# Kernel tuning notes

Hardware: AMD Instinct MI355X
Metric: run time of the kernel (lower is better)

The kernel has to match this reference:

```python
import math
import jax, jax.numpy as jnp
import numpy as np

HEADS = 8
DIM_HEAD = 64
NUM_MEM_KV = 16


def alibi_slopes(heads):
    def pow2_slopes(n):
        start = 2 ** (-(2 ** -(math.log2(n) - 3)))
        return [start * (start ** i) for i in range(n)]
    if math.log2(heads).is_integer():
        return np.asarray(pow2_slopes(heads), dtype=np.float32)
    cp2 = 2 ** math.floor(math.log2(heads))
    extra = pow2_slopes(2 * cp2)[0::2][: heads - cp2]
    return np.asarray(pow2_slopes(cp2) + extra, dtype=np.float32)


def setup_inputs() -> dict:
    key = jax.random.key(0)
    ks = jax.random.split(key, 12)
    b, n, dim = 2, 2048, 512
    h, dh, mem = HEADS, DIM_HEAD, NUM_MEM_KV
    s = 0.02  # weight init scale for numerical sanity
    return {
        "x": jax.random.normal(ks[0], (b, n, dim), jnp.float32),
        "Wq": jax.random.normal(ks[1], (dim, h * dh), jnp.float32) * s,
        "Wk": jax.random.normal(ks[2], (dim, h * dh), jnp.float32) * s,
        "Wv": jax.random.normal(ks[3], (dim, h * dh), jnp.float32) * s,
        "mem_k": jax.random.normal(ks[4], (h, mem, dh), jnp.float32),
        "mem_v": jax.random.normal(ks[5], (h, mem, dh), jnp.float32),
        "pre_proj": jax.random.normal(ks[6], (h, h), jnp.float32),
        "post_proj": jax.random.normal(ks[7], (h, h), jnp.float32),
        "head_scale_params": jnp.ones((1, h, 1, 1), jnp.float32),
        "Wout": jax.random.normal(ks[8], (h * dh, dim), jnp.float32) * s,
        "bout": jnp.zeros((dim,), jnp.float32),
    }


def reference(x, Wq, Wk, Wv, mem_k, mem_v, pre_proj, post_proj,
              head_scale_params, Wout, bout):
    b, n, dim = x.shape
    h, dh, mem = HEADS, DIM_HEAD, NUM_MEM_KV
    scale = dh ** -0.5

    def split_heads(t):  # [b,n,h*dh] -> [b,h,n,dh]
        return t.reshape(b, n, h, dh).transpose(0, 2, 1, 3)

    q = split_heads(x @ Wq)
    k = split_heads(x @ Wk)
    v = split_heads(x @ Wv)

    # prepend learned memory key/values: k,v -> [b,h,mem+n,dh]
    k = jnp.concatenate([jnp.broadcast_to(mem_k, (b, h, mem, dh)), k], axis=2)
    v = jnp.concatenate([jnp.broadcast_to(mem_v, (b, h, mem, dh)), v], axis=2)
    j = mem + n

    dots = jnp.einsum('bhid,bhjd->bhij', q, k) * scale
    # talking heads (pre-softmax)
    dots = jnp.einsum('bhij,hk->bkij', dots, pre_proj)
    # alibi relative positional bias: arange(j) * slope per head
    slopes = jnp.asarray(alibi_slopes(h))  # [h]
    dots = dots + jnp.arange(j, dtype=dots.dtype)[None, None, None, :] * slopes[None, :, None, None]
    # causal mask (mem columns always visible); mask where col-mem > row
    neg = -jnp.finfo(dots.dtype).max
    causal = (jnp.arange(j)[None, :] - mem) > jnp.arange(n)[:, None]  # [n,j]
    dots = jnp.where(causal[None, None], neg, dots)

    attn = jax.nn.softmax(dots, axis=-1)
    # talking heads (post-softmax)
    attn = jnp.einsum('bhij,hk->bkij', attn, post_proj)

    out = jnp.einsum('bhij,bhjd->bhid', attn, v)
    out = out * head_scale_params
    out = out.transpose(0, 2, 1, 3).reshape(b, n, h * dh)
    return out @ Wout + bout
```

## Files before the change

kernel.cpp:

```cpp
#include <hip/hip_runtime.h>
#include <math.h>

namespace {
constexpr int B = 2;
constexpr int N = 2048;
constexpr int DIM = 512;
constexpr int H = 8;
constexpr int MEM = 16;
constexpr int J = MEM + N;
constexpr int CHUNK = 256;
constexpr int CMAX = 9;
constexpr float S2 = 0.125f * 1.4426950408889634f;
constexpr size_t EPB = 17170432;
}

typedef __attribute__((ext_vector_type(8))) short short8;
typedef __attribute__((ext_vector_type(2))) float floatx2;
typedef __attribute__((ext_vector_type(4))) float floatx4;
typedef __attribute__((ext_vector_type(4))) unsigned short ushortx4;
typedef __attribute__((ext_vector_type(8))) unsigned short ushortx8;

__device__ inline unsigned short f2bf(float f) {
    unsigned int u = __float_as_uint(f);
    u += 0x7fffu + ((u >> 16) & 1u);
    return (unsigned short)(u >> 16);
}
__device__ inline unsigned int pk2bf(float a, float b) {
    return ((__float_as_uint(a) + 0x8000u) >> 16) |
           ((__float_as_uint(b) + 0x8000u) & 0xffff0000u);
}

__global__ __launch_bounds__(256)
void prep(const float* __restrict__ x,
          const float* __restrict__ Wq, const float* __restrict__ Wk,
          const float* __restrict__ Wv, const float* __restrict__ Wo,
          const float* __restrict__ mem_k, const float* __restrict__ mem_v,
          unsigned short* __restrict__ x16,
          unsigned short* __restrict__ tq, unsigned short* __restrict__ tk,
          unsigned short* __restrict__ tv, unsigned short* __restrict__ to_,
          unsigned short* __restrict__ k16, unsigned short* __restrict__ vt16,
          float* __restrict__ zbuf)
{
    __shared__ __align__(16) unsigned short tile[64][72];
    const int bid = blockIdx.x;
    const int t = threadIdx.x;

    if (bid < 1024) {
        const size_t base = ((size_t)bid * 256 + t) * 8;
        const float4 a = *(const float4*)(x + base);
        const float4 b = *(const float4*)(x + base + 4);
        ushortx8 o = { f2bf(a.x), f2bf(a.y), f2bf(a.z), f2bf(a.w),
                       f2bf(b.x), f2bf(b.y), f2bf(b.z), f2bf(b.w) };
        *(ushortx8*)(x16 + base) = o;
        return;
    }
    if (bid < 1280) {
        const int idx = bid - 1024;
        const int z = idx >> 6, rem = idx & 63;
        const float* __restrict__ W = (z == 0) ? Wq : (z == 1) ? Wk : (z == 2) ? Wv : Wo;
        unsigned short* __restrict__ WT = (z == 0) ? tq : (z == 1) ? tk : (z == 2) ? tv : to_;
        const int k0 = (rem >> 3) * 64, n0 = (rem & 7) * 64;

        const int rrow = t >> 4, rcol = (t & 15) * 4;
#pragma unroll
        for (int rr = 0; rr < 4; ++rr) {
            const int row = rrow + rr * 16;
            const float4 v = *(const float4*)(W + (size_t)(k0 + row) * DIM + n0 + rcol);
            tile[rcol + 0][row] = f2bf(v.x);
            tile[rcol + 1][row] = f2bf(v.y);
            tile[rcol + 2][row] = f2bf(v.z);
            tile[rcol + 3][row] = f2bf(v.w);
        }
        __syncthreads();
        const int orow = t >> 2, oseg = (t & 3) * 16;
        *(ushortx8*)(WT + (size_t)(n0 + orow) * DIM + k0 + oseg) =
            *(const ushortx8*)(&tile[orow][oseg]);
        *(ushortx8*)(WT + (size_t)(n0 + orow) * DIM + k0 + oseg + 8) =
            *(const ushortx8*)(&tile[orow][oseg + 8]);
        return;
    }
    if (bid < 1312) {
        const int idx = (bid - 1280) * 256 + t;
        if (idx >= H * MEM * 64) return;
        const int h0 = idx >> 10;
        const int rd = idx & 1023;
        const int r = rd >> 6, d = rd & 63;
        const unsigned short kk = f2bf(mem_k[idx]);
        const unsigned short vv = f2bf(mem_v[idx]);
#pragma unroll
        for (int bb = 0; bb < B; ++bb) {
            k16[((size_t)(bb * H + h0) * J + r) * 64 + d] = kk;
            vt16[((size_t)(bb * H + h0) * 64 + d) * J + r] = vv;
        }
        return;
    }
    {
        const size_t off = ((size_t)(bid - 1312) * 256 + t) * 4;
        *(float4*)(zbuf + off) = make_float4(0.f, 0.f, 0.f, 0.f);
    }
}

__global__ __launch_bounds__(256)
void qkv_gemm(const unsigned short* __restrict__ x16, const unsigned short* __restrict__ tq,
              const unsigned short* __restrict__ tk, const unsigned short* __restrict__ tv,
              unsigned short* __restrict__ q16, unsigned short* __restrict__ k16,
              unsigned short* __restrict__ vt16)
{
    const int which = blockIdx.z;
    const unsigned short* __restrict__ WT = (which == 0) ? tq : (which == 1) ? tk : tv;
    const int t = threadIdx.x;
    const int lane = t & 63, w = t >> 6;
    const int iL = lane & 15, quad = lane >> 4;
    const int mb = blockIdx.x * 64;
    const int n0 = blockIdx.y * 64;

    __shared__ __align__(16) unsigned short As[2][64][32];
    __shared__ __align__(16) unsigned short Bs[2][64][32];

    const int r0 = t >> 2, s8 = (t & 3) * 8;

    floatx4 acc[4];
#pragma unroll
    for (int ng = 0; ng < 4; ++ng) acc[ng] = (floatx4){0.f, 0.f, 0.f, 0.f};

    {
        *(ushortx8*)(&As[0][r0][s8]) =
            *(const ushortx8*)(x16 + (size_t)(mb + r0) * DIM + s8);
        *(ushortx8*)(&Bs[0][r0][s8]) =
            *(const ushortx8*)(WT + (size_t)(n0 + r0) * DIM + s8);
    }
    __syncthreads();

#pragma unroll
    for (int it = 0; it < 16; ++it) {
        const int buf = it & 1;
        if (it + 1 < 16) {
            const int k0 = (it + 1) * 32;
            const ushortx8 av = *(const ushortx8*)(x16 + (size_t)(mb + r0) * DIM + k0 + s8);
            const ushortx8 bv = *(const ushortx8*)(WT + (size_t)(n0 + r0) * DIM + k0 + s8);
            *(ushortx8*)(&As[buf ^ 1][r0][s8]) = av;
            *(ushortx8*)(&Bs[buf ^ 1][r0][s8]) = bv;
        }
        const short8 af = *(const short8*)(&As[buf][w * 16 + iL][quad * 8]);
#pragma unroll
        for (int ng = 0; ng < 4; ++ng) {
            const short8 bf = *(const short8*)(&Bs[buf][ng * 16 + iL][quad * 8]);
            acc[ng] = __builtin_amdgcn_mfma_f32_16x16x32_bf16(af, bf, acc[ng], 0, 0, 0);
        }
        __syncthreads();
    }

    const int mbw = mb + w * 16;
    const int h0 = n0 >> 6;
    if (which == 2) {
#pragma unroll
        for (int ng = 0; ng < 4; ++ng) {
            const int d = ng * 16 + iL;
#pragma unroll
            for (int r = 0; r < 4; ++r) {
                const int m = mbw + quad * 4 + r;
                const int bb = m >> 11, ii = m & (N - 1);
                vt16[((size_t)(bb * H + h0) * 64 + d) * J + MEM + ii] = f2bf(acc[ng][r]);
            }
        }
    } else {
        unsigned short* dst = (which == 0) ? q16 : k16;
#pragma unroll
        for (int ng = 0; ng < 4; ++ng) {
            const int d = ng * 16 + iL;
#pragma unroll
            for (int r = 0; r < 4; ++r) {
                const int m = mbw + quad * 4 + r;
                const int bb = m >> 11, ii = m & (N - 1);
                const size_t rowbase = (which == 0)
                    ? ((size_t)(bb * H + h0) * N + ii)
                    : ((size_t)(bb * H + h0) * J + MEM + ii);
                dst[rowbase * 64 + d] = f2bf(acc[ng][r]);
            }
        }
    }
}

__global__ __launch_bounds__(256)
void attn_scores(const unsigned short* __restrict__ qb, const unsigned short* __restrict__ kb,
                 const float* __restrict__ prep_p, float* __restrict__ lbuf,
                 unsigned short* __restrict__ e16)
{
    const int c = blockIdx.x, tt = 127 - blockIdx.y, b = blockIdx.z;
    const int i0 = tt * 16;
    const int jlim = i0 + 32;
    const int jstart = c * CHUNK;
    if (jstart >= jlim) return;
    const int jend = min(jstart + CHUNK, jlim);

    __shared__ __align__(16) unsigned short q_s[8][16][64];
    __shared__ __align__(16) float pre_s[64];
    const int t = threadIdx.x;
    if (t < 64) pre_s[t] = prep_p[t];
#pragma unroll
    for (int u4 = 0; u4 < 4; ++u4) {
        const int u = t + u4 * 256;
        const int h = u >> 7, rem = u & 127, i = rem >> 3, seg = (rem & 7) * 8;
        *(ushortx8*)(&q_s[h][i][seg]) =
            *(const ushortx8*)(qb + ((size_t)(b * H + h) * N + i0 + i) * 64 + seg);
    }
    __syncthreads();

    const int lane = t & 63, w = t >> 6;
    const int iL = lane & 15, quad = lane >> 4;
    const int i = i0 + iL;
    const size_t ebase = (size_t)b * EPB + (size_t)(8 * tt * tt + 24 * tt) * 128;

    float l_acc[8];
#pragma unroll
    for (int h1 = 0; h1 < 8; ++h1) l_acc[h1] = 0.f;

    bool any = false;
    for (int j0 = jstart + w * 16; j0 < jend; j0 += 64) {
        any = true;
        float dots[8][4];
#pragma unroll
        for (int h1 = 0; h1 < 8; ++h1)
#pragma unroll
            for (int r = 0; r < 4; ++r) dots[h1][r] = 0.f;

        const unsigned short* kp0 = kb + ((size_t)(b * H) * J + j0 + iL) * 64 + quad * 8;
        short8 kc0 = *(const short8*)kp0;
        short8 kc1 = *(const short8*)(kp0 + 32);
#pragma unroll
        for (int h0 = 0; h0 < 8; ++h0) {
            short8 kn0, kn1;
            if (h0 < 7) {
                const unsigned short* kpn =
                    kb + ((size_t)(b * H + h0 + 1) * J + j0 + iL) * 64 + quad * 8;
                kn0 = *(const short8*)kpn;
                kn1 = *(const short8*)(kpn + 32);
            }
            const short8 qf0 = *(const short8*)(&q_s[h0][iL][quad * 8]);
            const short8 qf1 = *(const short8*)(&q_s[h0][iL][quad * 8 + 32]);
            floatx4 a = {0.f, 0.f, 0.f, 0.f};
            a = __builtin_amdgcn_mfma_f32_16x16x32_bf16(kc0, qf0, a, 0, 0, 0);
            a = __builtin_amdgcn_mfma_f32_16x16x32_bf16(kc1, qf1, a, 0, 0, 0);
            const float4 pr0 = *(const float4*)(&pre_s[h0 * 8]);
            const float4 pr1 = *(const float4*)(&pre_s[h0 * 8 + 4]);
#pragma unroll
            for (int r = 0; r < 4; ++r) {
                const float av = a[r];
                dots[0][r] = fmaf(av, pr0.x, dots[0][r]);
                dots[1][r] = fmaf(av, pr0.y, dots[1][r]);
                dots[2][r] = fmaf(av, pr0.z, dots[2][r]);
                dots[3][r] = fmaf(av, pr0.w, dots[3][r]);
                dots[4][r] = fmaf(av, pr1.x, dots[4][r]);
                dots[5][r] = fmaf(av, pr1.y, dots[5][r]);
                dots[6][r] = fmaf(av, pr1.z, dots[6][r]);
                dots[7][r] = fmaf(av, pr1.w, dots[7][r]);
            }
            kc0 = kn0; kc1 = kn1;
        }

        unsigned int epk[4][4];
        float etmp[4];
#pragma unroll
        for (int h1 = 0; h1 < 8; ++h1) {
            const float slopeE = 1.4426950408889634f / (float)(2 << h1);
#pragma unroll
            for (int r = 0; r < 4; ++r) {
                const int j = j0 + quad * 4 + r;
                const bool vis = (j - MEM) <= i;
                const float e = vis ? exp2f(fmaf(dots[h1][r], S2, slopeE * (float)(j - i - MEM)))
                                    : 0.f;
                l_acc[h1] += e;
                if (h1 & 1) epk[r][h1 >> 1] = pk2bf(etmp[r], e);
                else        etmp[r] = e;
            }
        }
#pragma unroll
        for (int r = 0; r < 4; ++r) {
            uint4 o = make_uint4(epk[r][0], epk[r][1], epk[r][2], epk[r][3]);
            *(uint4*)(e16 + ebase + (size_t)((j0 + quad * 4 + r) * 16 + iL) * 8) = o;
        }
    }

#pragma unroll
    for (int h1 = 0; h1 < 8; ++h1) {
        float v = l_acc[h1];
        v += __shfl_xor(v, 16);
        v += __shfl_xor(v, 32);
        if (quad == 0 && any)
            atomicAdd(lbuf + ((size_t)(b * 128 + tt) * 8 + h1) * 16 + iL, v);
    }
}

__global__ __launch_bounds__(256)
void attn_pv2(const unsigned short* __restrict__ e16, const unsigned short* __restrict__ vt,
              const float* __restrict__ postp, const float* __restrict__ hsp,
              const float* __restrict__ lbuf, float* __restrict__ ao)
{
    const int c = blockIdx.x, tt = 127 - blockIdx.y, b = blockIdx.z;
    const int i0 = tt * 16;
    const int jlim = i0 + 32;
    const int jstart = c * CHUNK;
    if (jstart >= jlim) return;
    const int jend = min(jstart + CHUNK, jlim);
    const int nw = (jend - jstart + 31) >> 5;

    __shared__ __align__(16) unsigned short p2s[2][8][16][40];
    __shared__ __align__(16) float post_s[64];

    const int t = threadIdx.x;
    if (t < 64) post_s[t] = postp[t] * hsp[t & 7];

    const int lane = t & 63, w = t >> 6;
    const int iL = lane & 15, quad = lane >> 4;
    const int dW = w * 16 + iL;
    const int i_p = t & 15;
    const int jj = t >> 4;
    const size_t ebase = (size_t)b * EPB + (size_t)(8 * tt * tt + 24 * tt) * 128;
    const unsigned short* __restrict__ ep = e16 + ebase + (size_t)i_p * 8;

    float linv[8];
#pragma unroll
    for (int h1 = 0; h1 < 8; ++h1)
        linv[h1] = 1.0f / lbuf[((size_t)(b * 128 + tt) * 8 + h1) * 16 + i_p];

    floatx4 y[8];
#pragma unroll
    for (int h2 = 0; h2 < 8; ++h2) y[h2] = (floatx4){0.f, 0.f, 0.f, 0.f};

    ushortx8 evA[2], evB[2], evC[2];
    {
        const int j0c = jstart + jj * 2;
        int ja = min(j0c, jend - 1), jb2 = min(j0c + 1, jend - 1);
        evA[0] = *(const ushortx8*)(ep + (size_t)(ja * 16) * 8);
        evA[1] = *(const ushortx8*)(ep + (size_t)(jb2 * 16) * 8);
        ja = min(j0c + 32, jend - 1); jb2 = min(j0c + 33, jend - 1);
        evB[0] = *(const ushortx8*)(ep + (size_t)(ja * 16) * 8);
        evB[1] = *(const ushortx8*)(ep + (size_t)(jb2 * 16) * 8);
        ja = min(j0c + 64, jend - 1); jb2 = min(j0c + 65, jend - 1);
        evC[0] = *(const ushortx8*)(ep + (size_t)(ja * 16) * 8);
        evC[1] = *(const ushortx8*)(ep + (size_t)(jb2 * 16) * 8);
    }
    __syncthreads();

    for (int n = 0; n < nw; ++n) {
        const int jw0 = jstart + n * 32;
        const int buf = n & 1;

        int jbv = jw0 + quad * 8;
        if (jbv > J - 8) jbv = J - 8;
        short8 bF[8];
#pragma unroll
        for (int h2 = 0; h2 < 8; ++h2)
            bF[h2] = *(const short8*)(vt + ((size_t)(b * H + h2) * 64 + dW) * J + jbv);

        ushortx8 evT0, evT1;
        {
            const int wn = (n + 3 < nw) ? n + 3 : nw - 1;
            const int j0n = jstart + wn * 32 + jj * 2;
            const int ja = min(j0n, jend - 1), jb2 = min(j0n + 1, jend - 1);
            evT0 = *(const ushortx8*)(ep + (size_t)(ja * 16) * 8);
            evT1 = *(const ushortx8*)(ep + (size_t)(jb2 * 16) * 8);
        }

        floatx2 p2v[2][4];
#pragma unroll
        for (int s = 0; s < 2; ++s) {
#pragma unroll
            for (int q = 0; q < 4; ++q) p2v[s][q] = (floatx2){0.f, 0.f};
            const int j = jw0 + jj * 2 + s;
            if (j < jend) {
#pragma unroll
                for (int h1 = 0; h1 < 8; ++h1) {
                    const float e = __uint_as_float(
                        (unsigned int)(unsigned short)evA[s][h1] << 16) * linv[h1];
                    const floatx2* po = (const floatx2*)(&post_s[h1 * 8]);
                    p2v[s][0] += e * po[0];
                    p2v[s][1] += e * po[1];
                    p2v[s][2] += e * po[2];
                    p2v[s][3] += e * po[3];
                }
            }
        }
#pragma unroll
        for (int h2 = 0; h2 < 8; ++h2)
            *(unsigned int*)(&p2s[buf][h2][i_p][jj * 2]) =
                pk2bf(p2v[0][h2 >> 1][h2 & 1], p2v[1][h2 >> 1][h2 & 1]);
        __syncthreads();

#pragma unroll
        for (int h2 = 0; h2 < 8; ++h2) {
            const short8 aF = *(const short8*)(&p2s[buf][h2][iL][quad * 8]);
            y[h2] = __builtin_amdgcn_mfma_f32_16x16x32_bf16(aF, bF[h2], y[h2], 0, 0, 0);
        }
        evA[0] = evB[0]; evA[1] = evB[1];
        evB[0] = evC[0]; evB[1] = evC[1];
        evC[0] = evT0;   evC[1] = evT1;
    }

#pragma unroll
    for (int h2 = 0; h2 < 8; ++h2) {
#pragma unroll
        for (int r = 0; r < 4; ++r) {
            const int ii = i0 + quad * 4 + r;
            atomicAdd(ao + ((size_t)b * N + ii) * DIM + h2 * 64 + dW, y[h2][r]);
        }
    }
}

__global__ __launch_bounds__(256)
void out_gemm(const float* __restrict__ ain, const unsigned short* __restrict__ WT,
              const float* __restrict__ bo, float* __restrict__ out)
{
    const int t = threadIdx.x;
    const int lane = t & 63, w = t >> 6;
    const int iL = lane & 15, quad = lane >> 4;
    const int mb = blockIdx.x * 64;
    const int n0 = blockIdx.y * 64;

    __shared__ __align__(16) unsigned short As[2][64][32];
    __shared__ __align__(16) unsigned short Bs[2][64][32];

    const int ar0 = t >> 3, as4 = (t & 7) * 4;
    const int br0 = t >> 2, bs8 = (t & 3) * 8;

    floatx4 acc[4];
#pragma unroll
    for (int ng = 0; ng < 4; ++ng) acc[ng] = (floatx4){0.f, 0.f, 0.f, 0.f};

    {
        const float4 v0 = *(const float4*)(ain + (size_t)(mb + ar0) * DIM + as4);
        const float4 v1 = *(const float4*)(ain + (size_t)(mb + ar0 + 32) * DIM + as4);
        ushortx4 o0 = { f2bf(v0.x), f2bf(v0.y), f2bf(v0.z), f2bf(v0.w) };
        ushortx4 o1 = { f2bf(v1.x), f2bf(v1.y), f2bf(v1.z), f2bf(v1.w) };
        *(ushortx4*)(&As[0][ar0][as4]) = o0;
        *(ushortx4*)(&As[0][ar0 + 32][as4]) = o1;
        *(ushortx8*)(&Bs[0][br0][bs8]) =
            *(const ushortx8*)(WT + (size_t)(n0 + br0) * DIM + bs8);
    }
    __syncthreads();

#pragma unroll
    for (int it = 0; it < 16; ++it) {
        const int buf = it & 1;
        if (it + 1 < 16) {
            const int k0 = (it + 1) * 32;
            const float4 v0 = *(const float4*)(ain + (size_t)(mb + ar0) * DIM + k0 + as4);
            const float4 v1 = *(const float4*)(ain + (size_t)(mb + ar0 + 32) * DIM + k0 + as4);
            const ushortx8 bv =
                *(const ushortx8*)(WT + (size_t)(n0 + br0) * DIM + k0 + bs8);
            ushortx4 o0 = { f2bf(v0.x), f2bf(v0.y), f2bf(v0.z), f2bf(v0.w) };
            ushortx4 o1 = { f2bf(v1.x), f2bf(v1.y), f2bf(v1.z), f2bf(v1.w) };
            *(ushortx4*)(&As[buf ^ 1][ar0][as4]) = o0;
            *(ushortx4*)(&As[buf ^ 1][ar0 + 32][as4]) = o1;
            *(ushortx8*)(&Bs[buf ^ 1][br0][bs8]) = bv;
        }
        const short8 af = *(const short8*)(&As[buf][w * 16 + iL][quad * 8]);
#pragma unroll
        for (int ng = 0; ng < 4; ++ng) {
            const short8 bf = *(const short8*)(&Bs[buf][ng * 16 + iL][quad * 8]);
            acc[ng] = __builtin_amdgcn_mfma_f32_16x16x32_bf16(af, bf, acc[ng], 0, 0, 0);
        }
        __syncthreads();
    }

    const int mbw = mb + w * 16;
#pragma unroll
    for (int ng = 0; ng < 4; ++ng) {
        const int n = n0 + ng * 16 + iL;
        const float bias = bo[n];
#pragma unroll
        for (int r = 0; r < 4; ++r) {
            const int m = mbw + quad * 4 + r;
            out[(size_t)m * DIM + n] = acc[ng][r] + bias;
        }
    }
}

extern "C" void kernel_launch(void* const* d_in, const int* in_sizes, int n_in,
                              void* d_out, int out_size, void* d_ws, size_t ws_size,
                              hipStream_t stream)
{
    (void)in_sizes; (void)n_in; (void)out_size; (void)ws_size;
    const float* x      = (const float*)d_in[0];
    const float* Wq     = (const float*)d_in[1];
    const float* Wk     = (const float*)d_in[2];
    const float* Wv     = (const float*)d_in[3];
    const float* mem_k  = (const float*)d_in[4];
    const float* mem_v  = (const float*)d_in[5];
    const float* pre_p  = (const float*)d_in[6];
    const float* post_p = (const float*)d_in[7];
    const float* hs     = (const float*)d_in[8];
    const float* Wo     = (const float*)d_in[9];
    const float* bo     = (const float*)d_in[10];
    float* out = (float*)d_out;

    constexpr size_t NAO  = (size_t)B * N * DIM;
    constexpr size_t NLB  = (size_t)B * 128 * H * 16;
    constexpr size_t NW   = (size_t)DIM * DIM;
    constexpr size_t NQ   = (size_t)B * H * N * 64;
    constexpr size_t NK   = (size_t)B * H * J * 64;
    constexpr size_t NX   = (size_t)B * N * DIM;

    float* ws = (float*)d_ws;
    float* ao   = ws;
    float* lbuf = ao + NAO;
    unsigned short* wtq  = (unsigned short*)(lbuf + NLB);
    unsigned short* wtk  = wtq + NW;
    unsigned short* wtv  = wtk + NW;
    unsigned short* wto  = wtv + NW;
    unsigned short* q16  = wto + NW;
    unsigned short* k16  = q16 + NQ;
    unsigned short* v16  = k16 + NK;
    unsigned short* x16  = v16 + NK;
    unsigned short* e16  = x16 + NX;

    prep<<<dim3(3392), 256, 0, stream>>>(x, Wq, Wk, Wv, Wo, mem_k, mem_v,
                                         x16, wtq, wtk, wtv, wto, k16, v16, ao);
    qkv_gemm<<<dim3(64, 8, 3), 256, 0, stream>>>(x16, wtq, wtk, wtv, q16, k16, v16);
    attn_scores<<<dim3(CMAX, 128, B), 256, 0, stream>>>(q16, k16, pre_p, lbuf, e16);
    attn_pv2<<<dim3(CMAX, 128, B), 256, 0, stream>>>(e16, v16, post_p, hs, lbuf, ao);
    out_gemm<<<dim3(64, 8), 256, 0, stream>>>(ao, wto, bo, out);
}
```

Before: 221.5 us.

## Enlarge QKV and output GEMM tiles to 128x128 with direct global-to-LDS loads

The QKV and output projection GEMMs move from 64x64 tiles, where each wave holds a 16x64 strip, to 128x128 tiles where each wave computes a 64x64 sub-tile of 4x4 MFMAs. Operand staging uses global_load_lds to write straight into shared memory. The aim is more MFMA work per LDS fragment load and fewer redundant global reads. In exchange the grid drops to 384 and 128 blocks, so the 256 CUs are underfilled, and register pressure rises.

Result: slower. 237.1 us (+7.0%).

```diff
diff --git a/kernel.cpp b/kernel.cpp
--- a/kernel.cpp
+++ b/kernel.cpp
@@ -111,71 +111,77 @@
     const int t = threadIdx.x;
     const int lane = t & 63, w = t >> 6;
     const int iL = lane & 15, quad = lane >> 4;
-    const int mb = blockIdx.x * 64;
-    const int n0 = blockIdx.y * 64;
-
-    __shared__ __align__(16) unsigned short As[2][64][32];
-    __shared__ __align__(16) unsigned short Bs[2][64][32];
-
-    const int r0 = t >> 2, s8 = (t & 3) * 8;
-
-    floatx4 acc[4];
-#pragma unroll
-    for (int ng = 0; ng < 4; ++ng) acc[ng] = (floatx4){0.f, 0.f, 0.f, 0.f};
-
-    {
-        *(ushortx8*)(&As[0][r0][s8]) =
-            *(const ushortx8*)(x16 + (size_t)(mb + r0) * DIM + s8);
-        *(ushortx8*)(&Bs[0][r0][s8]) =
-            *(const ushortx8*)(WT + (size_t)(n0 + r0) * DIM + s8);
-    }
+    const int wr = w >> 1, wc = w & 1;
+    const int mb = blockIdx.x * 128;
+    const int n0 = blockIdx.y * 128;
+
+    __shared__ __align__(16) unsigned short As[2][128][32];
+    __shared__ __align__(16) unsigned short Bs[2][128][32];
+
+    const int srow = lane >> 2, scol = (lane & 3) * 8;
+
+    auto STAGE = [&](int buf, int k0) {
+#pragma unroll
+        for (int cc = 0; cc < 2; ++cc) {
+            const int rb = w * 32 + cc * 16;
+            const unsigned short* sa = x16 + (size_t)(mb + rb + srow) * DIM + k0 + scol;
+            __builtin_amdgcn_global_load_lds(
+                (const __attribute__((address_space(1))) unsigned int*)sa,
+                (__attribute__((address_space(3))) unsigned int*)(&As[buf][rb][0]),
+                16, 0, 0);
+            const unsigned short* sb = WT + (size_t)(n0 + rb + srow) * DIM + k0 + scol;
+            __builtin_amdgcn_global_load_lds(
+                (const __attribute__((address_space(1))) unsigned int*)sb,
+                (__attribute__((address_space(3))) unsigned int*)(&Bs[buf][rb][0]),
+                16, 0, 0);
+        }
+    };
+
+    floatx4 acc[4][4];
+#pragma unroll
+    for (int mi = 0; mi < 4; ++mi)
+#pragma unroll
+        for (int ni = 0; ni < 4; ++ni) acc[mi][ni] = (floatx4){0.f, 0.f, 0.f, 0.f};
+
+    STAGE(0, 0);
     __syncthreads();
 
-#pragma unroll
     for (int it = 0; it < 16; ++it) {
         const int buf = it & 1;
-        if (it + 1 < 16) {
-            const int k0 = (it + 1) * 32;
-            const ushortx8 av = *(const ushortx8*)(x16 + (size_t)(mb + r0) * DIM + k0 + s8);
-            const ushortx8 bv = *(const ushortx8*)(WT + (size_t)(n0 + r0) * DIM + k0 + s8);
-            *(ushortx8*)(&As[buf ^ 1][r0][s8]) = av;
-            *(ushortx8*)(&Bs[buf ^ 1][r0][s8]) = bv;
-        }
-        const short8 af = *(const short8*)(&As[buf][w * 16 + iL][quad * 8]);
-#pragma unroll
-        for (int ng = 0; ng < 4; ++ng) {
-            const short8 bf = *(const short8*)(&Bs[buf][ng * 16 + iL][quad * 8]);
-            acc[ng] = __builtin_amdgcn_mfma_f32_16x16x32_bf16(af, bf, acc[ng], 0, 0, 0);
-        }
+        if (it + 1 < 16) STAGE(buf ^ 1, (it + 1) * 32);
+        short8 aF[4], bF[4];
+#pragma unroll
+        for (int mi = 0; mi < 4; ++mi)
+            aF[mi] = *(const short8*)(&As[buf][wr * 64 + mi * 16 + iL][quad * 8]);
+#pragma unroll
+        for (int ni = 0; ni < 4; ++ni)
+            bF[ni] = *(const short8*)(&Bs[buf][wc * 64 + ni * 16 + iL][quad * 8]);
+#pragma unroll
+        for (int mi = 0; mi < 4; ++mi)
+#pragma unroll
+            for (int ni = 0; ni < 4; ++ni)
+                acc[mi][ni] = __builtin_amdgcn_mfma_f32_16x16x32_bf16(
+                    aF[mi], bF[ni], acc[mi][ni], 0, 0, 0);
         __syncthreads();
     }
 
-    const int mbw = mb + w * 16;
-    const int h0 = n0 >> 6;
-    if (which == 2) {
-#pragma unroll
-        for (int ng = 0; ng < 4; ++ng) {
-            const int d = ng * 16 + iL;
+#pragma unroll
+    for (int mi = 0; mi < 4; ++mi) {
+#pragma unroll
+        for (int ni = 0; ni < 4; ++ni) {
 #pragma unroll
             for (int r = 0; r < 4; ++r) {
-                const int m = mbw + quad * 4 + r;
+                const int m = mb + wr * 64 + mi * 16 + quad * 4 + r;
+                const int n = n0 + wc * 64 + ni * 16 + iL;
+                const int h0 = n >> 6, d = n & 63;
                 const int bb = m >> 11, ii = m & (N - 1);
-                vt16[((size_t)(bb * H + h0) * 64 + d) * J + MEM + ii] = f2bf(acc[ng][r]);
-            }
-        }
-    } else {
-        unsigned short* dst = (which == 0) ? q16 : k16;
-#pragma unroll
-        for (int ng = 0; ng < 4; ++ng) {
-            const int d = ng * 16 + iL;
-#pragma unroll
-            for (int r = 0; r < 4; ++r) {
-                const int m = mbw + quad * 4 + r;
-                const int bb = m >> 11, ii = m & (N - 1);
-                const size_t rowbase = (which == 0)
-                    ? ((size_t)(bb * H + h0) * N + ii)
-                    : ((size_t)(bb * H + h0) * J + MEM + ii);
-                dst[rowbase * 64 + d] = f2bf(acc[ng][r]);
+                const unsigned short v = f2bf(acc[mi][ni][r]);
+                if (which == 0)
+                    q16[((size_t)(bb * H + h0) * N + ii) * 64 + d] = v;
+                else if (which == 1)
+                    k16[((size_t)(bb * H + h0) * J + MEM + ii) * 64 + d] = v;
+                else
+                    vt16[((size_t)(bb * H + h0) * 64 + d) * J + MEM + ii] = v;
             }
         }
     }
@@ -414,64 +420,84 @@
     const int t = threadIdx.x;
     const int lane = t & 63, w = t >> 6;
     const int iL = lane & 15, quad = lane >> 4;
-    const int mb = blockIdx.x * 64;
-    const int n0 = blockIdx.y * 64;
-
-    __shared__ __align__(16) unsigned short As[2][64][32];
-    __shared__ __align__(16) unsigned short Bs[2][64][32];
-
-    const int ar0 = t >> 3, as4 = (t & 7) * 4;
-    const int br0 = t >> 2, bs8 = (t & 3) * 8;
-
-    floatx4 acc[4];
-#pragma unroll
-    for (int ng = 0; ng < 4; ++ng) acc[ng] = (floatx4){0.f, 0.f, 0.f, 0.f};
-
-    {
-        const float4 v0 = *(const float4*)(ain + (size_t)(mb + ar0) * DIM + as4);
-        const float4 v1 = *(const float4*)(ain + (size_t)(mb + ar0 + 32) * DIM + as4);
-        ushortx4 o0 = { f2bf(v0.x), f2bf(v0.y), f2bf(v0.z), f2bf(v0.w) };
-        ushortx4 o1 = { f2bf(v1.x), f2bf(v1.y), f2bf(v1.z), f2bf(v1.w) };
-        *(ushortx4*)(&As[0][ar0][as4]) = o0;
-        *(ushortx4*)(&As[0][ar0 + 32][as4]) = o1;
-        *(ushortx8*)(&Bs[0][br0][bs8]) =
-            *(const ushortx8*)(WT + (size_t)(n0 + br0) * DIM + bs8);
-    }
+    const int wr = w >> 1, wc = w & 1;
+    const int mb = blockIdx.x * 128;
+    const int n0 = blockIdx.y * 128;
+
+    __shared__ __align__(16) unsigned short As[2][128][32];
+    __shared__ __align__(16) unsigned short Bs[2][128][32];
+
+    const int ar = t >> 1, acb = (t & 1) * 16;
+    const int srow = lane >> 2, scol = (lane & 3) * 8;
+
+    auto STAGEA = [&](int buf, int k0) {
+        const float* src = ain + (size_t)(mb + ar) * DIM + k0 + acb;
+        const float4 v0 = *(const float4*)(src);
+        const float4 v1 = *(const float4*)(src + 4);
+        const float4 v2 = *(const float4*)(src + 8);
+        const float4 v3 = *(const float4*)(src + 12);
+        ushortx8 o0 = { f2bf(v0.x), f2bf(v0.y), f2bf(v0.z), f2bf(v0.w),
+                        f2bf(v1.x), f2bf(v1.y), f2bf(v1.z), f2bf(v1.w) };
+        ushortx8 o1 = { f2bf(v2.x), f2bf(v2.y), f2bf(v2.z), f2bf(v2.w),
+                        f2bf(v3.x), f2bf(v3.y), f2bf(v3.z), f2bf(v3.w) };
+        *(ushortx8*)(&As[buf][ar][acb]) = o0;
+        *(ushortx8*)(&As[buf][ar][acb + 8]) = o1;
+    };
+    auto STAGEB = [&](int buf, int k0) {
+#pragma unroll
+        for (int cc = 0; cc < 2; ++cc) {
+            const int rb = w * 32 + cc * 16;
+            const unsigned short* sb = WT + (size_t)(n0 + rb + srow) * DIM + k0 + scol;
+            __builtin_amdgcn_global_load_lds(
+                (const __attribute__((address_space(1))) unsigned int*)sb,
+                (__attribute__((address_space(3))) unsigned int*)(&Bs[buf][rb][0]),
+                16, 0, 0);
+        }
+    };
+
+    floatx4 acc[4][4];
+#pragma unroll
+    for (int mi = 0; mi < 4; ++mi)
+#pragma unroll
+        for (int ni = 0; ni < 4; ++ni) acc[mi][ni] = (floatx4){0.f, 0.f, 0.f, 0.f};
+
+    STAGEB(0, 0);
+    STAGEA(0, 0);
     __syncthreads();
 
-#pragma unroll
     for (int it = 0; it < 16; ++it) {
         const int buf = it & 1;
         if (it + 1 < 16) {
-            const int k0 = (it + 1) * 32;
-            const float4 v0 = *(const float4*)(ain + (size_t)(mb + ar0) * DIM + k0 + as4);
-            const float4 v1 = *(const float4*)(ain + (size_t)(mb + ar0 + 32) * DIM + k0 + as4);
-            const ushortx8 bv =
-                *(const ushortx8*)(WT + (size_t)(n0 + br0) * DIM + k0 + bs8);
-            ushortx4 o0 = { f2bf(v0.x), f2bf(v0.y), f2bf(v0.z), f2bf(v0.w) };
-            ushortx4 o1 = { f2bf(v1.x), f2bf(v1.y), f2bf(v1.z), f2bf(v1.w) };
-            *(ushortx4*)(&As[buf ^ 1][ar0][as4]) = o0;
-            *(ushortx4*)(&As[buf ^ 1][ar0 + 32][as4]) = o1;
-            *(ushortx8*)(&Bs[buf ^ 1][br0][bs8]) = bv;
-        }
-        const short8 af = *(const short8*)(&As[buf][w * 16 + iL][quad * 8]);
-#pragma unroll
-        for (int ng = 0; ng < 4; ++ng) {
-            const short8 bf = *(const short8*)(&Bs[buf][ng * 16 + iL][quad * 8]);
-            acc[ng] = __builtin_amdgcn_mfma_f32_16x16x32_bf16(af, bf, acc[ng], 0, 0, 0);
-        }
+            STAGEB(buf ^ 1, (it + 1) * 32);
+            STAGEA(buf ^ 1, (it + 1) * 32);
+        }
+        short8 aF[4], bF[4];
+#pragma unroll
+        for (int mi = 0; mi < 4; ++mi)
+            aF[mi] = *(const short8*)(&As[buf][wr * 64 + mi * 16 + iL][quad * 8]);
+#pragma unroll
+        for (int ni = 0; ni < 4; ++ni)
+            bF[ni] = *(const short8*)(&Bs[buf][wc * 64 + ni * 16 + iL][quad * 8]);
+#pragma unroll
+        for (int mi = 0; mi < 4; ++mi)
+#pragma unroll
+            for (int ni = 0; ni < 4; ++ni)
+                acc[mi][ni] = __builtin_amdgcn_mfma_f32_16x16x32_bf16(
+                    aF[mi], bF[ni], acc[mi][ni], 0, 0, 0);
         __syncthreads();
     }
 
-    const int mbw = mb + w * 16;
-#pragma unroll
-    for (int ng = 0; ng < 4; ++ng) {
-        const int n = n0 + ng * 16 + iL;
-        const float bias = bo[n];
-#pragma unroll
-        for (int r = 0; r < 4; ++r) {
-            const int m = mbw + quad * 4 + r;
-            out[(size_t)m * DIM + n] = acc[ng][r] + bias;
+#pragma unroll
+    for (int mi = 0; mi < 4; ++mi) {
+#pragma unroll
+        for (int ni = 0; ni < 4; ++ni) {
+            const int n = n0 + wc * 64 + ni * 16 + iL;
+            const float bias = bo[n];
+#pragma unroll
+            for (int r = 0; r < 4; ++r) {
+                const int m = mb + wr * 64 + mi * 16 + quad * 4 + r;
+                out[(size_t)m * DIM + n] = acc[mi][ni][r] + bias;
+            }
         }
     }
 }
@@ -516,8 +542,8 @@
 
     prep<<<dim3(3392), 256, 0, stream>>>(x, Wq, Wk, Wv, Wo, mem_k, mem_v,
                                          x16, wtq, wtk, wtv, wto, k16, v16, ao);
-    qkv_gemm<<<dim3(64, 8, 3), 256, 0, stream>>>(x16, wtq, wtk, wtv, q16, k16, v16);
+    qkv_gemm<<<dim3(32, 4, 3), 256, 0, stream>>>(x16, wtq, wtk, wtv, q16, k16, v16);
     attn_scores<<<dim3(CMAX, 128, B), 256, 0, stream>>>(q16, k16, pre_p, lbuf, e16);
     attn_pv2<<<dim3(CMAX, 128, B), 256, 0, stream>>>(e16, v16, post_p, hs, lbuf, ao);
-    out_gemm<<<dim3(64, 8), 256, 0, stream>>>(ao, wto, bo, out);
-}
+    out_gemm<<<dim3(32, 4), 256, 0, stream>>>(ao, wto, bo, out);
+}
```
